# Performance work log

Measured on AMD Instinct MI355X. Metric: run time of the kernel, lower is better.

## Reference

```python
import jax, jax.numpy as jnp
import numpy as np
from jax import lax

N = 2048
BS = 64
NUM_ITR = 25


def setup_inputs() -> dict:
    key = jax.random.key(0)
    k1, k2, k3, k4, k5 = jax.random.split(key, 5)
    scale = 0.5 / np.sqrt(N)  # keep iteration matrices contractive so the recurrence stays bounded
    H = jax.random.normal(k1, (N, N), dtype=jnp.float32) / np.sqrt(N)
    Dinv = jax.random.normal(k2, (N, N), dtype=jnp.float32) * scale
    U = jax.random.normal(k3, (N, N), dtype=jnp.float32) * scale
    invM = jax.random.normal(k4, (N, N), dtype=jnp.float32) * scale
    y = jax.random.normal(k5, (BS, N), dtype=jnp.float32)
    return {"num_itr": NUM_ITR, "bs": BS, "y": y, "H": H, "Dinv": Dinv, "U": U, "invM": invM}


def reference(num_itr, bs, y, H, Dinv, U, invM):
    n = H.shape[0]
    s0 = jnp.zeros((bs, n), dtype=y.dtype)
    yMF = y @ H.T                 # [bs, n]
    s_init = yMF @ Dinv           # initial Gauss-Seidel estimate

    def step(s, _):
        s_next = (yMF - s @ U) @ invM
        return s_next, s_next

    s_final, traj_iters = lax.scan(step, s_init, None, length=num_itr)
    # traj matches the torch list: [zeros, s_1, ..., s_num_itr]
    traj = jnp.concatenate([s0[None], traj_iters], axis=0)  # [num_itr+1, bs, n]
    return s_final, traj
```

## Files before the change

kernel.cpp:

```cpp
#include <hip/hip_runtime.h>
#include <hip/hip_bf16.h>

#define NDIM 2048
#define BS   64
#define NM4  (NDIM * NDIM / 4)
#define BSN  ((size_t)BS * NDIM)
#define SMEM_BYTES 69632

typedef __bf16 bf16_t;
typedef __bf16 bf16x4 __attribute__((ext_vector_type(4)));
typedef __bf16 bf16x8 __attribute__((ext_vector_type(8)));
typedef float  f32x4  __attribute__((ext_vector_type(4)));

__device__ __forceinline__ void gload16(const void* g, void* lds) {
  __builtin_amdgcn_global_load_lds(
      (const __attribute__((address_space(1))) void*)g,
      (__attribute__((address_space(3))) void*)lds, 16, 0, 0);
}
__device__ __forceinline__ uint32_t lds_off(void* p) {
  return (uint32_t)(uintptr_t)(__attribute__((address_space(3))) void*)p;
}

#define WB4 asm volatile("s_waitcnt vmcnt(4)\n\ts_barrier" ::: "memory")
#define WB2 asm volatile("s_waitcnt vmcnt(2)\n\ts_barrier" ::: "memory")
#define WB0 asm volatile("s_waitcnt vmcnt(0)\n\ts_barrier" ::: "memory")

__global__ __launch_bounds__(512) void prep(
    const float* __restrict__ H, const float* __restrict__ U,
    const float* __restrict__ Dinv, const float* __restrict__ invM,
    const float* __restrict__ y,
    bf16_t* __restrict__ H16, bf16_t* __restrict__ U16,
    bf16_t* __restrict__ Dt, bf16_t* __restrict__ iMt,
    bf16_t* __restrict__ y16, float* __restrict__ traj0) {
  __shared__ bf16_t tile[64][72];
  int b = blockIdx.x, tid = threadIdx.x;
  if (b < 1024) {
#pragma unroll
    for (int i = 0; i < 4; ++i) {
      int idx = b * 2048 + i * 512 + tid;
      const float* src = (idx < NM4) ? H : U;
      bf16_t* dst = (idx < NM4) ? H16 : U16;
      int j = (idx < NM4) ? idx : idx - NM4;
      float4 v = ((const float4*)src)[j];
      bf16x4 o = {(bf16_t)v.x, (bf16_t)v.y, (bf16_t)v.z, (bf16_t)v.w};
      ((bf16x4*)dst)[j] = o;
    }
    int yi = b * 512 + tid;
    if (yi < BS * NDIM / 4) {
      float4 w = ((const float4*)y)[yi];
      bf16x4 o2 = {(bf16_t)w.x, (bf16_t)w.y, (bf16_t)w.z, (bf16_t)w.w};
      ((bf16x4*)y16)[yi] = o2;
      ((float4*)traj0)[yi] = make_float4(0.f, 0.f, 0.f, 0.f);
    }
  } else {
    int id = b - 1024;
    const float* src = (id < 1024) ? Dinv : invM;
    bf16_t* dst = (id < 1024) ? Dt : iMt;
    id &= 1023;
    int bx = id & 31, by = id >> 5;
    int r = tid >> 3, c8 = (tid & 7) * 8;
    const float* sp = src + (size_t)(by * 64 + r) * NDIM + bx * 64 + c8;
    float4 v0 = *(const float4*)sp;
    float4 v1 = *(const float4*)(sp + 4);
    bf16_t* t = &tile[r][c8];
    t[0] = (bf16_t)v0.x; t[1] = (bf16_t)v0.y; t[2] = (bf16_t)v0.z; t[3] = (bf16_t)v0.w;
    t[4] = (bf16_t)v1.x; t[5] = (bf16_t)v1.y; t[6] = (bf16_t)v1.z; t[7] = (bf16_t)v1.w;
    __syncthreads();
    bf16x8 o;
#pragma unroll
    for (int j = 0; j < 8; ++j) o[j] = tile[c8 + j][r];
    *(bf16x8*)(dst + (size_t)(bx * 64 + r) * NDIM + by * 64 + c8) = o;
  }
}

__device__ __forceinline__ void wgemm_role(
    const bf16_t* __restrict__ A, const bf16_t* __restrict__ Bt,
    bf16_t* __restrict__ C, bf16_t* __restrict__ Ct, int blk, char* smem) {
  int tid = threadIdx.x, lane = tid & 63, wave = tid >> 6;
  int m0 = (blk >> 4) * 128, n0 = (blk & 15) * 128;
  int rl = lane & 15, q = lane >> 4;
  const bf16_t* Ag = A  + (size_t)(m0 + wave * 16 + rl) * NDIM + q * 8;
  const bf16_t* Bg = Bt + (size_t)(n0 + wave * 16 + rl) * NDIM + q * 8;
  char* ldsA = smem + wave * 1024;
  char* ldsB = smem + 8192 + wave * 1024;

  int wr2 = (wave & 3) * 2, wc4 = (wave >> 2) * 4;
  uint32_t abase = lds_off(smem) + wr2 * 1024 + lane * 16;
  uint32_t bbase = lds_off(smem) + 8192 + wc4 * 1024 + lane * 16;

  f32x4 acc[2][4];
#pragma unroll
  for (int i = 0; i < 2; ++i)
#pragma unroll
    for (int j = 0; j < 4; ++j) acc[i][j] = (f32x4){0.f, 0.f, 0.f, 0.f};

#define STAGE(s)                                  \
  {                                               \
    int _b = (s) & 3, _k = (s) * 32;              \
    gload16(Ag + _k, ldsA + _b * 16384);          \
    gload16(Bg + _k, ldsB + _b * 16384);          \
  }
#define COMPUTE(bb)                                                            \
  {                                                                            \
    uint32_t av = abase + (bb) * 16384;                                        \
    uint32_t bv = bbase + (bb) * 16384;                                        \
    bf16x8 af0, af1, bg0, bg1, bg2, bg3;                                       \
    asm volatile("ds_read_b128 %0, %1"             : "=v"(af0) : "v"(av));     \
    asm volatile("ds_read_b128 %0, %1 offset:1024" : "=v"(af1) : "v"(av));     \
    asm volatile("ds_read_b128 %0, %1"             : "=v"(bg0) : "v"(bv));     \
    asm volatile("ds_read_b128 %0, %1 offset:1024" : "=v"(bg1) : "v"(bv));     \
    asm volatile("ds_read_b128 %0, %1 offset:2048" : "=v"(bg2) : "v"(bv));     \
    asm volatile("ds_read_b128 %0, %1 offset:3072" : "=v"(bg3) : "v"(bv));     \
    asm volatile("s_waitcnt lgkmcnt(0)"                                        \
                 : "+v"(af0), "+v"(af1), "+v"(bg0), "+v"(bg1), "+v"(bg2),      \
                   "+v"(bg3));                                                 \
    acc[0][0] = __builtin_amdgcn_mfma_f32_16x16x32_bf16(af0, bg0, acc[0][0], 0, 0, 0); \
    acc[0][1] = __builtin_amdgcn_mfma_f32_16x16x32_bf16(af0, bg1, acc[0][1], 0, 0, 0); \
    acc[0][2] = __builtin_amdgcn_mfma_f32_16x16x32_bf16(af0, bg2, acc[0][2], 0, 0, 0); \
    acc[0][3] = __builtin_amdgcn_mfma_f32_16x16x32_bf16(af0, bg3, acc[0][3], 0, 0, 0); \
    acc[1][0] = __builtin_amdgcn_mfma_f32_16x16x32_bf16(af1, bg0, acc[1][0], 0, 0, 0); \
    acc[1][1] = __builtin_amdgcn_mfma_f32_16x16x32_bf16(af1, bg1, acc[1][1], 0, 0, 0); \
    acc[1][2] = __builtin_amdgcn_mfma_f32_16x16x32_bf16(af1, bg2, acc[1][2], 0, 0, 0); \
    acc[1][3] = __builtin_amdgcn_mfma_f32_16x16x32_bf16(af1, bg3, acc[1][3], 0, 0, 0); \
  }

  STAGE(0); STAGE(1); STAGE(2);
  int s = 3;
#pragma unroll 1
  for (int k = 0; k < 60; k += 4) {
    WB4; STAGE(s); ++s; COMPUTE(0);
    WB4; STAGE(s); ++s; COMPUTE(1);
    WB4; STAGE(s); ++s; COMPUTE(2);
    WB4; STAGE(s); ++s; COMPUTE(3);
  }
  WB4; STAGE(63); COMPUTE(0);
  WB4; COMPUTE(1);
  WB2; COMPUTE(2);
  WB0; COMPUTE(3);
#undef STAGE
#undef COMPUTE

#pragma unroll
  for (int i = 0; i < 2; ++i)
#pragma unroll
    for (int j = 0; j < 4; ++j)
#pragma unroll
      for (int r = 0; r < 4; ++r)
        C[(size_t)(m0 + (wr2 + i) * 16 + q * 4 + r) * NDIM + n0 + (wc4 + j) * 16 + rl] =
            (bf16_t)acc[i][j][r];

  if (Ct) {
    __syncthreads();
    bf16_t (*tileT)[136] = (bf16_t(*)[136])smem;
#pragma unroll
    for (int i = 0; i < 2; ++i)
#pragma unroll
      for (int j = 0; j < 4; ++j)
#pragma unroll
        for (int r = 0; r < 4; ++r)
          tileT[(wc4 + j) * 16 + rl][(wr2 + i) * 16 + q * 4 + r] = (bf16_t)acc[i][j][r];
    __syncthreads();
#pragma unroll
    for (int t = 0; t < 4; ++t) {
      int v = t * 512 + tid, row = v >> 4, c8 = (v & 15) * 8;
      *(bf16x8*)(Ct + (size_t)(n0 + row) * NDIM + m0 + c8) = *(bf16x8*)&tileT[row][c8];
    }
  }
}

__device__ __forceinline__ void skinny_role(
    const bf16_t* __restrict__ A, const bf16_t* __restrict__ Bt, int n0, char* smem,
    const float* __restrict__ add, float sign,
    float* o32, float* o32b, bf16_t* o16) {
  int tid = threadIdx.x, lane = tid & 63, wave = tid >> 6;
  int rl = lane & 15, q = lane >> 4;
#pragma unroll
  for (int i = 0; i < 8; ++i) {
    const bf16_t* g = Bt + (size_t)(n0 + rl) * NDIM + (i * 8 + wave) * 32 + q * 8;
    gload16(g, smem + (size_t)(i * 512 + wave * 64) * 16);
  }
  __syncthreads();

  int ms = (wave & 3) * 16, kh = wave >> 2;
  const bf16x8* Ap = (const bf16x8*)(A + (size_t)(ms + rl) * NDIM) + q + kh * 128;
  const bf16x8* Bp = (const bf16x8*)smem + lane + kh * 2048;

  f32x4 acc[8];
#pragma unroll
  for (int i = 0; i < 8; ++i) acc[i] = (f32x4){0.f, 0.f, 0.f, 0.f};
#pragma unroll
  for (int c = 0; c < 32; ++c)
    acc[c & 7] = __builtin_amdgcn_mfma_f32_16x16x32_bf16(Ap[c * 4], Bp[c * 64], acc[c & 7], 0, 0, 0);
  f32x4 s = ((acc[0] + acc[1]) + (acc[2] + acc[3])) + ((acc[4] + acc[5]) + (acc[6] + acc[7]));

  f32x4* red = (f32x4*)(smem + 65536);
  if (wave >= 4) red[(wave & 3) * 64 + lane] = s;
  __syncthreads();
  if (wave < 4) {
    s += red[wave * 64 + lane];
    int mrow = ms + q * 4, col = n0 + rl;
#pragma unroll
    for (int r = 0; r < 4; ++r) {
      size_t o = (size_t)(mrow + r) * NDIM + col;
      float v = sign * s[r];
      if (add) v += add[o];
      if (o32)  o32[o]  = v;
      if (o32b) o32b[o] = v;
      if (o16)  o16[o]  = (bf16_t)v;
    }
  }
}

__global__ __launch_bounds__(512, 4) void megaA(
    const bf16_t* __restrict__ U16, const bf16_t* __restrict__ iMt16,
    const bf16_t* __restrict__ y16, const bf16_t* __restrict__ H16,
    bf16_t* __restrict__ Wrm, bf16_t* __restrict__ Wt, bf16_t* __restrict__ yMF16) {
  __shared__ char smem[SMEM_BYTES];
  int b = blockIdx.x;
  if (b < 256) wgemm_role(U16, iMt16, Wrm, Wt, b, smem);
  else         skinny_role(y16, H16, (b - 256) * 16, smem, nullptr, 1.f, nullptr, nullptr, yMF16);
}

__global__ __launch_bounds__(512, 4) void megaB(
    const bf16_t* __restrict__ yMF16, const bf16_t* __restrict__ iMt16,
    const bf16_t* __restrict__ Dt16,
    float* __restrict__ c32, bf16_t* __restrict__ c16, bf16_t* __restrict__ z0) {
  __shared__ char smem[SMEM_BYTES];
  int b = blockIdx.x;
  if (b < 128) skinny_role(yMF16, iMt16, b * 16, smem, nullptr, 1.f, c32, nullptr, c16);
  else         skinny_role(yMF16, Dt16, (b - 128) * 16, smem, nullptr, 1.f, nullptr, nullptr, z0);
}

__global__ __launch_bounds__(512, 4) void megaC(
    const bf16_t* __restrict__ Wt, const bf16_t* __restrict__ Wrm,
    const bf16_t* __restrict__ z0, const bf16_t* __restrict__ c16,
    const float* __restrict__ c32,
    bf16_t* __restrict__ W2t, bf16_t* __restrict__ W2rm,
    float* __restrict__ traj1, bf16_t* __restrict__ z0b,
    float* __restrict__ c2_32, bf16_t* __restrict__ c2_16) {
  __shared__ char smem[SMEM_BYTES];
  int b = blockIdx.x;
  if (b < 256)      wgemm_role(Wt, Wrm, W2t, W2rm, b, smem);
  else if (b < 384) skinny_role(z0, Wt, (b - 256) * 16, smem, c32, -1.f, traj1, nullptr, z0b);
  else              skinny_role(c16, Wt, (b - 384) * 16, smem, c32, -1.f, c2_32, nullptr, c2_16);
}

__global__ __launch_bounds__(512, 4) void megaD(
    const bf16_t* __restrict__ W2t, const bf16_t* __restrict__ z0,
    const bf16_t* __restrict__ c2_16, const float* __restrict__ c2_32,
    float* __restrict__ traj2, float* __restrict__ traj3,
    bf16_t* __restrict__ zA, float* __restrict__ c4_32) {
  __shared__ char smem[SMEM_BYTES];
  int b = blockIdx.x;
  if (b < 128)      skinny_role(z0, W2t, b * 16, smem, c2_32, 1.f, traj2, nullptr, zA);
  else if (b < 256) skinny_role(z0 + BSN, W2t, (b - 128) * 16, smem, c2_32, 1.f, traj3, nullptr, zA + BSN);
  else              skinny_role(c2_16, W2t, (b - 256) * 16, smem, c2_32, 1.f, c4_32, nullptr, nullptr);
}

__global__ __launch_bounds__(512, 4) void megaE(
    const bf16_t* __restrict__ W2t, const bf16_t* __restrict__ W2rm,
    const bf16_t* __restrict__ zA_in, const float* __restrict__ c2_32,
    bf16_t* __restrict__ W4t, float* __restrict__ traj4, float* __restrict__ traj5,
    bf16_t* __restrict__ zA) {
  __shared__ char smem[SMEM_BYTES];
  int b = blockIdx.x;
  if (b < 256)      wgemm_role(W2t, W2rm, W4t, nullptr, b, smem);
  else if (b < 384) skinny_role(zA_in, W2t, (b - 256) * 16, smem, c2_32, 1.f, traj4, nullptr, zA + 2 * BSN);
  else              skinny_role(zA_in + BSN, W2t, (b - 384) * 16, smem, c2_32, 1.f, traj5, nullptr, zA + 3 * BSN);
}

__global__ __launch_bounds__(512, 4) void quad_step(
    const bf16_t* __restrict__ zin, const bf16_t* __restrict__ W4t,
    const float* __restrict__ c4_32, float* __restrict__ trajb,
    bf16_t* __restrict__ zout, float* __restrict__ sfin) {
  __shared__ char smem[SMEM_BYTES];
  int b = blockIdx.x, ci = b & 3, p = b >> 2;
  skinny_role(zin + (size_t)ci * BSN, W4t, p * 16, smem, c4_32, 1.f,
              trajb + (size_t)ci * BSN, (ci == 3) ? sfin : nullptr,
              zout + (size_t)ci * BSN);
}

extern "C" void kernel_launch(void* const* d_in, const int* in_sizes, int n_in,
                              void* d_out, int out_size, void* d_ws, size_t ws_size,
                              hipStream_t stream) {
  const float* y    = (const float*)d_in[2];
  const float* H    = (const float*)d_in[3];
  const float* Dinv = (const float*)d_in[4];
  const float* U    = (const float*)d_in[5];
  const float* invM = (const float*)d_in[6];

  float* out     = (float*)d_out;
  float* s_final = out;
  float* traj    = out + BSN;

  char* ws = (char*)d_ws;
  size_t off = 0;
  auto alloc = [&](size_t bytes) -> void* {
    void* p = ws + off;
    off += (bytes + 255) & ~(size_t)255;
    return p;
  };
  bf16_t* U16   = (bf16_t*)alloc((size_t)NDIM * NDIM * 2);
  bf16_t* Dt16  = (bf16_t*)alloc((size_t)NDIM * NDIM * 2);
  bf16_t* iMt16 = (bf16_t*)alloc((size_t)NDIM * NDIM * 2);
  bf16_t* H16   = (bf16_t*)alloc((size_t)NDIM * NDIM * 2);
  bf16_t* Wrm   = (bf16_t*)alloc((size_t)NDIM * NDIM * 2);
  bf16_t* Wt    = (bf16_t*)alloc((size_t)NDIM * NDIM * 2);
  bf16_t* y16   = (bf16_t*)alloc(BSN * 2);
  bf16_t* yMF16 = (bf16_t*)alloc(BSN * 2);
  bf16_t* c16   = (bf16_t*)alloc(BSN * 2);
  bf16_t* c2_16 = (bf16_t*)alloc(BSN * 2);
  float*  c32   = (float*)alloc(BSN * 4);
  float*  c2_32 = (float*)alloc(BSN * 4);
  float*  c4_32 = (float*)alloc(BSN * 4);
  bf16_t* z0    = (bf16_t*)alloc(2 * BSN * 2);
  bf16_t* zA    = (bf16_t*)alloc(4 * BSN * 2);
  bf16_t* zB    = (bf16_t*)alloc(4 * BSN * 2);
  bf16_t* W2t   = H16;
  bf16_t* W2rm  = U16;
  bf16_t* W4t   = Dt16;

  prep<<<3072, 512, 0, stream>>>(H, U, Dinv, invM, y, H16, U16, Dt16, iMt16, y16, traj);
  megaA<<<384, 512, 0, stream>>>(U16, iMt16, y16, H16, Wrm, Wt, yMF16);
  megaB<<<256, 512, 0, stream>>>(yMF16, iMt16, Dt16, c32, c16, z0);
  megaC<<<512, 512, 0, stream>>>(Wt, Wrm, z0, c16, c32, W2t, W2rm,
                                 traj + BSN, z0 + BSN, c2_32, c2_16);
  megaD<<<384, 512, 0, stream>>>(W2t, z0, c2_16, c2_32, traj + 2 * BSN, traj + 3 * BSN,
                                 zA, c4_32);
  megaE<<<512, 512, 0, stream>>>(W2t, W2rm, zA, c2_32, W4t, traj + 4 * BSN, traj + 5 * BSN, zA);

  bf16_t* zcur = zA;
  bf16_t* znxt = zB;
  for (int g = 0; g < 5; ++g) {
    float* sfin = (g == 4) ? s_final : nullptr;
    quad_step<<<512, 512, 0, stream>>>(zcur, W4t, c4_32, traj + (size_t)(6 + 4 * g) * BSN,
                                       znxt, sfin);
    bf16_t* tmp = zcur; zcur = znxt; znxt = tmp;
  }
}
```

Baseline: 385.2 us.

## Deepen wide-GEMM prefetch to six LDS stages and swizzle block-to-tile mapping

The 2048x2048 bf16 GEMM role goes from a 4-buffer to a 6-buffer global-to-LDS pipeline, keeping four stages in flight instead of three. This needs 96KB of shared memory in the GEMM-hosting kernels, so their launch bounds drop to 2 blocks per CU. Block indices are also remapped so neighbouring blocks work on 4x4 groups of tiles, aiming at better L2 reuse of A and B rows. The cost is lower occupancy, which also applies to the skinny roles fused into those same kernels.

```diff
diff --git a/kernel.cpp b/kernel.cpp
--- a/kernel.cpp
+++ b/kernel.cpp
@@ -5,7 +5,8 @@
 #define BS   64
 #define NM4  (NDIM * NDIM / 4)
 #define BSN  ((size_t)BS * NDIM)
-#define SMEM_BYTES 69632
+#define SMEM_HEAVY 98304
+#define SMEM_LIGHT 69632
 
 typedef __bf16 bf16_t;
 typedef __bf16 bf16x4 __attribute__((ext_vector_type(4)));
@@ -21,9 +22,7 @@
   return (uint32_t)(uintptr_t)(__attribute__((address_space(3))) void*)p;
 }
 
-#define WB4 asm volatile("s_waitcnt vmcnt(4)\n\ts_barrier" ::: "memory")
-#define WB2 asm volatile("s_waitcnt vmcnt(2)\n\ts_barrier" ::: "memory")
-#define WB0 asm volatile("s_waitcnt vmcnt(0)\n\ts_barrier" ::: "memory")
+#define WBN(n) asm volatile("s_waitcnt vmcnt(" #n ")\n\ts_barrier" ::: "memory")
 
 __global__ __launch_bounds__(512) void prep(
     const float* __restrict__ H, const float* __restrict__ U,
@@ -77,7 +76,12 @@
     const bf16_t* __restrict__ A, const bf16_t* __restrict__ Bt,
     bf16_t* __restrict__ C, bf16_t* __restrict__ Ct, int blk, char* smem) {
   int tid = threadIdx.x, lane = tid & 63, wave = tid >> 6;
-  int m0 = (blk >> 4) * 128, n0 = (blk & 15) * 128;
+  int x = blk & 7, j = blk >> 3;
+  int t = x * 2 + (j >> 4);
+  int mi = (j >> 2) & 3, ni = j & 3;
+  int m0 = ((t >> 2) * 4 + mi) * 128;
+  int n0 = ((t & 3) * 4 + ni) * 128;
+
   int rl = lane & 15, q = lane >> 4;
   const bf16_t* Ag = A  + (size_t)(m0 + wave * 16 + rl) * NDIM + q * 8;
   const bf16_t* Bg = Bt + (size_t)(n0 + wave * 16 + rl) * NDIM + q * 8;
@@ -92,13 +96,13 @@
 #pragma unroll
   for (int i = 0; i < 2; ++i)
 #pragma unroll
-    for (int j = 0; j < 4; ++j) acc[i][j] = (f32x4){0.f, 0.f, 0.f, 0.f};
-
-#define STAGE(s)                                  \
+    for (int jj = 0; jj < 4; ++jj) acc[i][jj] = (f32x4){0.f, 0.f, 0.f, 0.f};
+
+#define STAGE(buf, s)                             \
   {                                               \
-    int _b = (s) & 3, _k = (s) * 32;              \
-    gload16(Ag + _k, ldsA + _b * 16384);          \
-    gload16(Bg + _k, ldsB + _b * 16384);          \
+    int _k = (s) * 32;                            \
+    gload16(Ag + _k, ldsA + (buf) * 16384);       \
+    gload16(Bg + _k, ldsB + (buf) * 16384);       \
   }
 #define COMPUTE(bb)                                                            \
   {                                                                            \
@@ -124,30 +128,38 @@
     acc[1][3] = __builtin_amdgcn_mfma_f32_16x16x32_bf16(af1, bg3, acc[1][3], 0, 0, 0); \
   }
 
-  STAGE(0); STAGE(1); STAGE(2);
-  int s = 3;
+  STAGE(0, 0); STAGE(1, 1); STAGE(2, 2); STAGE(3, 3); STAGE(4, 4);
 #pragma unroll 1
-  for (int k = 0; k < 60; k += 4) {
-    WB4; STAGE(s); ++s; COMPUTE(0);
-    WB4; STAGE(s); ++s; COMPUTE(1);
-    WB4; STAGE(s); ++s; COMPUTE(2);
-    WB4; STAGE(s); ++s; COMPUTE(3);
-  }
-  WB4; STAGE(63); COMPUTE(0);
-  WB4; COMPUTE(1);
-  WB2; COMPUTE(2);
-  WB0; COMPUTE(3);
+  for (int g = 0; g < 9; ++g) {
+    int i = g * 6;
+    WBN(8); STAGE(5, i + 5);  COMPUTE(0);
+    WBN(8); STAGE(0, i + 6);  COMPUTE(1);
+    WBN(8); STAGE(1, i + 7);  COMPUTE(2);
+    WBN(8); STAGE(2, i + 8);  COMPUTE(3);
+    WBN(8); STAGE(3, i + 9);  COMPUTE(4);
+    WBN(8); STAGE(4, i + 10); COMPUTE(5);
+  }
+  WBN(8); STAGE(5, 59); COMPUTE(0);
+  WBN(8); STAGE(0, 60); COMPUTE(1);
+  WBN(8); STAGE(1, 61); COMPUTE(2);
+  WBN(8); STAGE(2, 62); COMPUTE(3);
+  WBN(8); STAGE(3, 63); COMPUTE(4);
+  WBN(8); COMPUTE(5);
+  WBN(6); COMPUTE(0);
+  WBN(4); COMPUTE(1);
+  WBN(2); COMPUTE(2);
+  WBN(0); COMPUTE(3);
 #undef STAGE
 #undef COMPUTE
 
 #pragma unroll
   for (int i = 0; i < 2; ++i)
 #pragma unroll
-    for (int j = 0; j < 4; ++j)
+    for (int jj = 0; jj < 4; ++jj)
 #pragma unroll
       for (int r = 0; r < 4; ++r)
-        C[(size_t)(m0 + (wr2 + i) * 16 + q * 4 + r) * NDIM + n0 + (wc4 + j) * 16 + rl] =
-            (bf16_t)acc[i][j][r];
+        C[(size_t)(m0 + (wr2 + i) * 16 + q * 4 + r) * NDIM + n0 + (wc4 + jj) * 16 + rl] =
+            (bf16_t)acc[i][jj][r];
 
   if (Ct) {
     __syncthreads();
@@ -155,14 +167,14 @@
 #pragma unroll
     for (int i = 0; i < 2; ++i)
 #pragma unroll
-      for (int j = 0; j < 4; ++j)
+      for (int jj = 0; jj < 4; ++jj)
 #pragma unroll
         for (int r = 0; r < 4; ++r)
-          tileT[(wc4 + j) * 16 + rl][(wr2 + i) * 16 + q * 4 + r] = (bf16_t)acc[i][j][r];
+          tileT[(wc4 + jj) * 16 + rl][(wr2 + i) * 16 + q * 4 + r] = (bf16_t)acc[i][jj][r];
     __syncthreads();
 #pragma unroll
-    for (int t = 0; t < 4; ++t) {
-      int v = t * 512 + tid, row = v >> 4, c8 = (v & 15) * 8;
+    for (int tt = 0; tt < 4; ++tt) {
+      int v = tt * 512 + tid, row = v >> 4, c8 = (v & 15) * 8;
       *(bf16x8*)(Ct + (size_t)(n0 + row) * NDIM + m0 + c8) = *(bf16x8*)&tileT[row][c8];
     }
   }
@@ -211,11 +223,11 @@
   }
 }
 
-__global__ __launch_bounds__(512, 4) void megaA(
+__global__ __launch_bounds__(512, 2) void megaA(
     const bf16_t* __restrict__ U16, const bf16_t* __restrict__ iMt16,
     const bf16_t* __restrict__ y16, const bf16_t* __restrict__ H16,
     bf16_t* __restrict__ Wrm, bf16_t* __restrict__ Wt, bf16_t* __restrict__ yMF16) {
-  __shared__ char smem[SMEM_BYTES];
+  __shared__ char smem[SMEM_HEAVY];
   int b = blockIdx.x;
   if (b < 256) wgemm_role(U16, iMt16, Wrm, Wt, b, smem);
   else         skinny_role(y16, H16, (b - 256) * 16, smem, nullptr, 1.f, nullptr, nullptr, yMF16);
@@ -225,20 +237,20 @@
     const bf16_t* __restrict__ yMF16, const bf16_t* __restrict__ iMt16,
     const bf16_t* __restrict__ Dt16,
     float* __restrict__ c32, bf16_t* __restrict__ c16, bf16_t* __restrict__ z0) {
-  __shared__ char smem[SMEM_BYTES];
+  __shared__ char smem[SMEM_LIGHT];
   int b = blockIdx.x;
   if (b < 128) skinny_role(yMF16, iMt16, b * 16, smem, nullptr, 1.f, c32, nullptr, c16);
   else         skinny_role(yMF16, Dt16, (b - 128) * 16, smem, nullptr, 1.f, nullptr, nullptr, z0);
 }
 
-__global__ __launch_bounds__(512, 4) void megaC(
+__global__ __launch_bounds__(512, 2) void megaC(
     const bf16_t* __restrict__ Wt, const bf16_t* __restrict__ Wrm,
     const bf16_t* __restrict__ z0, const bf16_t* __restrict__ c16,
     const float* __restrict__ c32,
     bf16_t* __restrict__ W2t, bf16_t* __restrict__ W2rm,
     float* __restrict__ traj1, bf16_t* __restrict__ z0b,
     float* __restrict__ c2_32, bf16_t* __restrict__ c2_16) {
-  __shared__ char smem[SMEM_BYTES];
+  __shared__ char smem[SMEM_HEAVY];
   int b = blockIdx.x;
   if (b < 256)      wgemm_role(Wt, Wrm, W2t, W2rm, b, smem);
   else if (b < 384) skinny_role(z0, Wt, (b - 256) * 16, smem, c32, -1.f, traj1, nullptr, z0b);
@@ -250,19 +262,19 @@
     const bf16_t* __restrict__ c2_16, const float* __restrict__ c2_32,
     float* __restrict__ traj2, float* __restrict__ traj3,
     bf16_t* __restrict__ zA, float* __restrict__ c4_32) {
-  __shared__ char smem[SMEM_BYTES];
+  __shared__ char smem[SMEM_LIGHT];
   int b = blockIdx.x;
   if (b < 128)      skinny_role(z0, W2t, b * 16, smem, c2_32, 1.f, traj2, nullptr, zA);
   else if (b < 256) skinny_role(z0 + BSN, W2t, (b - 128) * 16, smem, c2_32, 1.f, traj3, nullptr, zA + BSN);
   else              skinny_role(c2_16, W2t, (b - 256) * 16, smem, c2_32, 1.f, c4_32, nullptr, nullptr);
 }
 
-__global__ __launch_bounds__(512, 4) void megaE(
+__global__ __launch_bounds__(512, 2) void megaE(
     const bf16_t* __restrict__ W2t, const bf16_t* __restrict__ W2rm,
     const bf16_t* __restrict__ zA_in, const float* __restrict__ c2_32,
     bf16_t* __restrict__ W4t, float* __restrict__ traj4, float* __restrict__ traj5,
     bf16_t* __restrict__ zA) {
-  __shared__ char smem[SMEM_BYTES];
+  __shared__ char smem[SMEM_HEAVY];
   int b = blockIdx.x;
   if (b < 256)      wgemm_role(W2t, W2rm, W4t, nullptr, b, smem);
   else if (b < 384) skinny_role(zA_in, W2t, (b - 256) * 16, smem, c2_32, 1.f, traj4, nullptr, zA + 2 * BSN);
@@ -273,7 +285,7 @@
     const bf16_t* __restrict__ zin, const bf16_t* __restrict__ W4t,
     const float* __restrict__ c4_32, float* __restrict__ trajb,
     bf16_t* __restrict__ zout, float* __restrict__ sfin) {
-  __shared__ char smem[SMEM_BYTES];
+  __shared__ char smem[SMEM_LIGHT];
   int b = blockIdx.x, ci = b & 3, p = b >> 2;
   skinny_role(zin + (size_t)ci * BSN, W4t, p * 16, smem, c4_32, 1.f,
               trajb + (size_t)ci * BSN, (ci == 3) ? sfin : nullptr,
```

New measurement: 390.5 us. Within noise of the previous version (+1.4%).
